# Kernel tuning notes

Measured on AMD Instinct MI355X. Metric: run time of the kernel, lower is better.

Reference implementation:

```python
import jax, jax.numpy as jnp
import numpy as np

N_NODES = 100000
N_EDGES = 3200000
IN_DIM, HID_DIM, N_CLASS = 64, 32, 20


def setup_inputs() -> dict:
    key = jax.random.key(0)
    k1, k2, k3, k4, k5, k6 = jax.random.split(key, 6)
    x = jax.random.normal(k1, (N_NODES, IN_DIM), dtype=jnp.float32)
    edge_index = jax.random.randint(k2, (2, N_EDGES), 0, N_NODES, dtype=jnp.int64)
    W1 = jax.random.normal(k3, (IN_DIM, HID_DIM), dtype=jnp.float32) / np.sqrt(IN_DIM)
    b1 = jnp.zeros((HID_DIM,), dtype=jnp.float32)
    Wout = jax.random.normal(k4, (HID_DIM, N_CLASS), dtype=jnp.float32) / np.sqrt(HID_DIM)
    bout = jnp.zeros((N_CLASS,), dtype=jnp.float32)
    return {"x": x, "edge_index": edge_index, "W1": W1, "b1": b1, "Wout": Wout, "bout": bout}


def gcn_conv(x, edge_index, W, b):
    # PyG GCNConv defaults: add self-loops, symmetric deg^{-1/2} normalization.
    n = x.shape[0]
    loop = jnp.arange(n, dtype=edge_index.dtype)
    row = jnp.concatenate([edge_index[0], loop])  # source
    col = jnp.concatenate([edge_index[1], loop])  # target
    deg = jax.ops.segment_sum(jnp.ones_like(col, dtype=x.dtype), col, num_segments=n)
    dis = jnp.where(deg > 0, deg ** -0.5, 0.0)
    norm = dis[row] * dis[col]  # [E+N]
    xw = x @ W  # [N, HID]
    msg = norm[:, None] * xw[row]  # [E+N, HID]
    agg = jax.ops.segment_sum(msg, col, num_segments=n)
    return agg + b


def reference(x, edge_index, W1, b1, Wout, bout):
    h = gcn_conv(x, edge_index, W1, b1)
    emb = jax.nn.relu(h)
    return emb @ Wout + bout
```

## Files before the change

kernel.cpp:

```cpp
#include <hip/hip_runtime.h>
#include <hip/hip_fp16.h>
#include <math.h>

#define N_NODES 100000
#define N_EDGES 3200000
#define IN_DIM 64
#define HID_DIM 32
#define N_CLASS 20

#define BKT_BITS 6
#define BKT_W    64
#define NBKT     1563
#define CAP_BKT  2560
#define HALF_W   32
#define CAP_D    1536
#define CHUNK    4096
#define EPT      16
#define NBLK_E   ((N_EDGES + CHUNK - 1) / CHUNK)
#define ENT_R    (CAP_BKT / 256)

__global__ void k_detect(const int* __restrict__ ei32, int* __restrict__ flag,
                         int* __restrict__ gcursor) {
    __shared__ int any;
    if (threadIdx.x == 0) any = 0;
    __syncthreads();
    int nz = 0;
    for (int k = threadIdx.x; k < 4096; k += blockDim.x)
        if (ei32[2 * k + 1] != 0) nz = 1;
    if (nz) atomicOr(&any, 1);
    for (int i = threadIdx.x; i < NBKT; i += blockDim.x) gcursor[i] = i * CAP_BKT;
    __syncthreads();
    if (threadIdx.x == 0) *flag = any ? 0 : 1;
}

__device__ __forceinline__ int get_idx(const int* __restrict__ ei32, int wide, int pos) {
    return wide ? ei32[2 * (long long)pos] : ei32[pos];
}

__global__ void __launch_bounds__(256, 8)
kC_scatter(const int* __restrict__ ei32, const int* __restrict__ flag,
           int* __restrict__ gcursor, unsigned int* __restrict__ pk) {
    __shared__ int lh[NBKT];
    __shared__ int lgb[NBKT];
    __shared__ int lrt[NBKT];
    int wide = *flag;
    for (int i = threadIdx.x; i < NBKT; i += blockDim.x) { lh[i] = 0; lrt[i] = 0; }
    __syncthreads();
    int base = blockIdx.x * CHUNK;
    int src[EPT], dst[EPT];
#pragma unroll
    for (int k = 0; k < EPT; ++k) {
        int e = base + k * 256 + threadIdx.x;
        if (e < N_EDGES) {
            src[k] = get_idx(ei32, wide, e);
            dst[k] = get_idx(ei32, wide, N_EDGES + e);
            atomicAdd(&lh[dst[k] >> BKT_BITS], 1);
        } else dst[k] = -1;
    }
    __syncthreads();
    for (int b = threadIdx.x; b < NBKT; b += blockDim.x)
        if (lh[b]) lgb[b] = atomicAdd(&gcursor[b], lh[b]);
    __syncthreads();
#pragma unroll
    for (int k = 0; k < EPT; ++k) {
        if (dst[k] >= 0) {
            int b = dst[k] >> BKT_BITS;
            int r = atomicAdd(&lrt[b], 1);
            int pos = lgb[b] + r;
            if (pos < (b + 1) * CAP_BKT)
                pk[pos] = ((unsigned)src[k] << BKT_BITS) | (unsigned)(dst[k] & (BKT_W - 1));
        }
    }
}

__global__ void kC1_deg(const unsigned int* __restrict__ pk, const int* __restrict__ gcursor,
                        float* __restrict__ dis) {
    __shared__ int lcnt[BKT_W];
    int b = blockIdx.x;
    int gb = b * CAP_BKT;
    int bsz = min(gcursor[b] - gb, CAP_BKT);
    if (threadIdx.x < BKT_W) lcnt[threadIdx.x] = 0;
    __syncthreads();
    for (int i = threadIdx.x; i < bsz; i += blockDim.x)
        atomicAdd(&lcnt[pk[gb + i] & (BKT_W - 1)], 1);
    __syncthreads();
    int node = b * BKT_W + threadIdx.x;
    if (threadIdx.x < BKT_W && node < N_NODES)
        dis[node] = rsqrtf((float)(lcnt[threadIdx.x] + 1));
}

__global__ void k_xw(const float* __restrict__ x, const float* __restrict__ W1,
                     const float* __restrict__ dis, __half* __restrict__ xw16) {
    __shared__ float sW[IN_DIM * HID_DIM];
    for (int i = threadIdx.x; i < IN_DIM * HID_DIM; i += blockDim.x) sW[i] = W1[i];
    __syncthreads();
    int tid = blockIdx.x * blockDim.x + threadIdx.x;
    int node = tid >> 3;
    int q = tid & 7;
    if (node >= N_NODES) return;
    const float4* xr = reinterpret_cast<const float4*>(x + (size_t)node * IN_DIM);
    float4 a = make_float4(0.f, 0.f, 0.f, 0.f);
#pragma unroll
    for (int k4 = 0; k4 < IN_DIM / 4; ++k4) {
        float4 xv = xr[k4];
        const float4 w0 = *reinterpret_cast<const float4*>(&sW[(k4 * 4 + 0) * HID_DIM + q * 4]);
        const float4 w1 = *reinterpret_cast<const float4*>(&sW[(k4 * 4 + 1) * HID_DIM + q * 4]);
        const float4 w2 = *reinterpret_cast<const float4*>(&sW[(k4 * 4 + 2) * HID_DIM + q * 4]);
        const float4 w3 = *reinterpret_cast<const float4*>(&sW[(k4 * 4 + 3) * HID_DIM + q * 4]);
        a.x += xv.x * w0.x + xv.y * w1.x + xv.z * w2.x + xv.w * w3.x;
        a.y += xv.x * w0.y + xv.y * w1.y + xv.z * w2.y + xv.w * w3.y;
        a.z += xv.x * w0.z + xv.y * w1.z + xv.z * w2.z + xv.w * w3.z;
        a.w += xv.x * w0.w + xv.y * w1.w + xv.z * w2.w + xv.w * w3.w;
    }
    float d = dis[node];
    union { __half2 h2[2]; uint2 u; } cvt;
    cvt.h2[0] = __floats2half2_rn(a.x * d, a.y * d);
    cvt.h2[1] = __floats2half2_rn(a.z * d, a.w * d);
    *reinterpret_cast<uint2*>(xw16 + (size_t)node * HID_DIM + q * 4) = cvt.u;
}

__device__ __forceinline__ void acc_row(float4& acc, uint2 u) {
    union U { unsigned u; __half2 hh; };
    U a0; a0.u = u.x; U a1; a1.u = u.y;
    float2 f0 = __half22float2(a0.hh);
    float2 f1 = __half22float2(a1.hh);
    acc.x += f0.x; acc.y += f0.y; acc.z += f1.x; acc.w += f1.y;
}

__global__ void __launch_bounds__(256, 8)
kD_gather(const unsigned int* __restrict__ pk, const int* __restrict__ gcursor,
          const float* __restrict__ dis, const __half* __restrict__ xw16,
          const float* __restrict__ b1, const float* __restrict__ Wout,
          const float* __restrict__ bout, float* __restrict__ out) {
    __shared__ int   ssrc[CAP_D];
    __shared__ int   lcnt[HALF_W], lstart[HALF_W], lrt[HALF_W];
    __shared__ int   stot;
    __shared__ float sW[HID_DIM * N_CLASS];
    __shared__ float sb1[HID_DIM];
    __shared__ float sbo[N_CLASS];
    for (int i = threadIdx.x; i < HID_DIM * N_CLASS; i += blockDim.x) sW[i] = Wout[i];
    if (threadIdx.x < HID_DIM) sb1[threadIdx.x] = b1[threadIdx.x];
    if (threadIdx.x < N_CLASS) sbo[threadIdx.x] = bout[threadIdx.x];
    if (threadIdx.x < HALF_W) { lcnt[threadIdx.x] = 0; lrt[threadIdx.x] = 0; }
    int B = blockIdx.x;
    int b = B >> 1, h = B & 1;
    int gb = b * CAP_BKT;
    int bsz = min(gcursor[b] - gb, CAP_BKT);
    __syncthreads();

    unsigned ents[ENT_R];
#pragma unroll
    for (int i = 0; i < ENT_R; ++i) {
        int idx = i * 256 + (int)threadIdx.x;
        ents[i] = (idx < bsz) ? pk[gb + idx] : 0xFFFFFFFFu;
    }
#pragma unroll
    for (int i = 0; i < ENT_R; ++i) {
        if (ents[i] != 0xFFFFFFFFu) {
            int ld = (int)(ents[i] & (BKT_W - 1));
            if ((ld >> 5) == h) atomicAdd(&lcnt[ld & (HALF_W - 1)], 1);
        }
    }
    __syncthreads();
    if (threadIdx.x < HALF_W) {
        int v = lcnt[threadIdx.x];
        int s = v;
#pragma unroll
        for (int d = 1; d < HALF_W; d <<= 1) {
            int t = __shfl_up(s, d, HALF_W);
            if ((int)(threadIdx.x & (HALF_W - 1)) >= d) s += t;
        }
        lstart[threadIdx.x] = s - v;
        if (threadIdx.x == HALF_W - 1) stot = s;
    }
    __syncthreads();
    bool fits = (stot <= CAP_D);
    if (fits) {
#pragma unroll
        for (int i = 0; i < ENT_R; ++i) {
            if (ents[i] != 0xFFFFFFFFu) {
                int ld = (int)(ents[i] & (BKT_W - 1));
                if ((ld >> 5) == h) {
                    int r = atomicAdd(&lrt[ld & (HALF_W - 1)], 1);
                    ssrc[lstart[ld & (HALF_W - 1)] + r] = (int)(ents[i] >> BKT_BITS);
                }
            }
        }
    }
    __syncthreads();

    int grp = threadIdx.x >> 3, part = threadIdx.x & 7;
    int ln = grp;
    int node = b * BKT_W + h * HALF_W + ln;
    if (node >= N_NODES) return;

    float4 acc = make_float4(0.f, 0.f, 0.f, 0.f);
    acc_row(acc, *reinterpret_cast<const uint2*>(xw16 + (size_t)node * HID_DIM + part * 4));
    float dc = dis[node];

    if (fits) {
        int s0 = lstart[ln], cnt = lcnt[ln];
        int e = s0, end = s0 + cnt;
        while (e + 8 <= end) {
            int srcs[8];
#pragma unroll
            for (int j = 0; j < 8; ++j) srcs[j] = ssrc[e + j];
            uint2 us[8];
#pragma unroll
            for (int j = 0; j < 8; ++j)
                us[j] = *reinterpret_cast<const uint2*>(xw16 + (size_t)srcs[j] * HID_DIM + part * 4);
#pragma unroll
            for (int j = 0; j < 8; ++j) acc_row(acc, us[j]);
            e += 8;
        }
        for (; e < end; ++e) {
            int src = ssrc[e];
            acc_row(acc, *reinterpret_cast<const uint2*>(xw16 + (size_t)src * HID_DIM + part * 4));
        }
    } else {
        int want = h * HALF_W + ln;
        for (int i = 0; i < bsz; ++i) {
            unsigned v = pk[gb + i];
            if ((int)(v & (BKT_W - 1)) == want)
                acc_row(acc, *reinterpret_cast<const uint2*>(xw16 + (size_t)(v >> BKT_BITS) * HID_DIM + part * 4));
        }
    }
    float e0 = fmaxf(dc * acc.x + sb1[part * 4 + 0], 0.f);
    float e1 = fmaxf(dc * acc.y + sb1[part * 4 + 1], 0.f);
    float e2 = fmaxf(dc * acc.z + sb1[part * 4 + 2], 0.f);
    float e3 = fmaxf(dc * acc.w + sb1[part * 4 + 3], 0.f);
    float o[N_CLASS];
#pragma unroll
    for (int cl = 0; cl < N_CLASS; ++cl) {
        o[cl] = e0 * sW[(part * 4 + 0) * N_CLASS + cl]
              + e1 * sW[(part * 4 + 1) * N_CLASS + cl]
              + e2 * sW[(part * 4 + 2) * N_CLASS + cl]
              + e3 * sW[(part * 4 + 3) * N_CLASS + cl];
    }
#pragma unroll
    for (int m = 1; m < 8; m <<= 1) {
#pragma unroll
        for (int cl = 0; cl < N_CLASS; ++cl) o[cl] += __shfl_xor(o[cl], m, 64);
    }
    if (part < 5) {
        float4 w = make_float4(o[part * 4 + 0] + sbo[part * 4 + 0],
                               o[part * 4 + 1] + sbo[part * 4 + 1],
                               o[part * 4 + 2] + sbo[part * 4 + 2],
                               o[part * 4 + 3] + sbo[part * 4 + 3]);
        *reinterpret_cast<float4*>(out + (size_t)node * N_CLASS + part * 4) = w;
    }
}

extern "C" void kernel_launch(void* const* d_in, const int* in_sizes, int n_in,
                              void* d_out, int out_size, void* d_ws, size_t ws_size,
                              hipStream_t stream) {
    const float* x    = (const float*)d_in[0];
    const int*   ei32 = (const int*)d_in[1];
    const float* W1   = (const float*)d_in[2];
    const float* b1   = (const float*)d_in[3];
    const float* Wout = (const float*)d_in[4];
    const float* bout = (const float*)d_in[5];
    float* out = (float*)d_out;

    __half*       xw16    = (__half*)d_ws;
    unsigned int* pk      = (unsigned int*)((char*)d_ws + (size_t)N_NODES * HID_DIM * 2);
    int*          gcursor = (int*)(pk + (size_t)NBKT * CAP_BKT);
    float*        dis     = (float*)(gcursor + NBKT);
    int*          flag    = (int*)(dis + N_NODES);

    k_detect<<<1, 256, 0, stream>>>(ei32, flag, gcursor);
    kC_scatter<<<NBLK_E, 256, 0, stream>>>(ei32, flag, gcursor, pk);
    kC1_deg<<<NBKT, 256, 0, stream>>>(pk, gcursor, dis);
    k_xw<<<(N_NODES * 8 + 255) / 256, 256, 0, stream>>>(x, W1, dis, xw16);
    kD_gather<<<2 * NBKT, 256, 0, stream>>>(pk, gcursor, dis, xw16, b1, Wout, bout, out);
}
```

Before: 137.5 us.

## Split edge bucketing into two-pass radix scatter via coarse super-buckets

```diff
diff --git a/kernel.cpp b/kernel.cpp
--- a/kernel.cpp
+++ b/kernel.cpp
@@ -14,13 +14,18 @@
 #define CAP_BKT  2560
 #define HALF_W   32
 #define CAP_D    1536
-#define CHUNK    4096
-#define EPT      16
-#define NBLK_E   ((N_EDGES + CHUNK - 1) / CHUNK)
 #define ENT_R    (CAP_BKT / 256)
 
+#define SUP_SHIFT 12
+#define NS       25
+#define CAP_S    132000
+#define CH1      2048
+#define NBLK1    ((N_EDGES + CH1 - 1) / CH1)
+#define CH2      4096
+#define BPS      ((CAP_S + CH2 - 1) / CH2)
+
 __global__ void k_detect(const int* __restrict__ ei32, int* __restrict__ flag,
-                         int* __restrict__ gcursor) {
+                         int* __restrict__ scursor, int* __restrict__ gcursor) {
     __shared__ int any;
     if (threadIdx.x == 0) any = 0;
     __syncthreads();
@@ -29,6 +34,7 @@
         if (ei32[2 * k + 1] != 0) nz = 1;
     if (nz) atomicOr(&any, 1);
     for (int i = threadIdx.x; i < NBKT; i += blockDim.x) gcursor[i] = i * CAP_BKT;
+    if (threadIdx.x < NS) scursor[threadIdx.x] = threadIdx.x * CAP_S;
     __syncthreads();
     if (threadIdx.x == 0) *flag = any ? 0 : 1;
 }
@@ -37,38 +43,78 @@
     return wide ? ei32[2 * (long long)pos] : ei32[pos];
 }
 
-__global__ void __launch_bounds__(256, 8)
-kC_scatter(const int* __restrict__ ei32, const int* __restrict__ flag,
-           int* __restrict__ gcursor, unsigned int* __restrict__ pk) {
-    __shared__ int lh[NBKT];
-    __shared__ int lgb[NBKT];
-    __shared__ int lrt[NBKT];
+__global__ void __launch_bounds__(512, 4)
+kS1(const int* __restrict__ ei32, const int* __restrict__ flag,
+    int* __restrict__ scursor, unsigned int* __restrict__ sp) {
+    __shared__ int lh[NS], lgb[NS], lrt[NS];
     int wide = *flag;
-    for (int i = threadIdx.x; i < NBKT; i += blockDim.x) { lh[i] = 0; lrt[i] = 0; }
-    __syncthreads();
-    int base = blockIdx.x * CHUNK;
-    int src[EPT], dst[EPT];
-#pragma unroll
-    for (int k = 0; k < EPT; ++k) {
-        int e = base + k * 256 + threadIdx.x;
+    if (threadIdx.x < NS) { lh[threadIdx.x] = 0; lrt[threadIdx.x] = 0; }
+    __syncthreads();
+    int base = blockIdx.x * CH1;
+    int src[4], dst[4];
+#pragma unroll
+    for (int k = 0; k < 4; ++k) {
+        int e = base + k * 512 + (int)threadIdx.x;
         if (e < N_EDGES) {
             src[k] = get_idx(ei32, wide, e);
             dst[k] = get_idx(ei32, wide, N_EDGES + e);
-            atomicAdd(&lh[dst[k] >> BKT_BITS], 1);
+            atomicAdd(&lh[dst[k] >> SUP_SHIFT], 1);
         } else dst[k] = -1;
     }
     __syncthreads();
-    for (int b = threadIdx.x; b < NBKT; b += blockDim.x)
-        if (lh[b]) lgb[b] = atomicAdd(&gcursor[b], lh[b]);
-    __syncthreads();
-#pragma unroll
-    for (int k = 0; k < EPT; ++k) {
+    if (threadIdx.x < NS && lh[threadIdx.x])
+        lgb[threadIdx.x] = atomicAdd(&scursor[threadIdx.x], lh[threadIdx.x]);
+    __syncthreads();
+#pragma unroll
+    for (int k = 0; k < 4; ++k) {
         if (dst[k] >= 0) {
-            int b = dst[k] >> BKT_BITS;
-            int r = atomicAdd(&lrt[b], 1);
-            int pos = lgb[b] + r;
+            int s = dst[k] >> SUP_SHIFT;
+            int r = atomicAdd(&lrt[s], 1);
+            int pos = lgb[s] + r;
+            if (pos < (s + 1) * CAP_S)
+                sp[pos] = ((unsigned)src[k] << SUP_SHIFT) |
+                          (unsigned)(dst[k] & ((1 << SUP_SHIFT) - 1));
+        }
+    }
+}
+
+__global__ void __launch_bounds__(512, 4)
+kS2(const unsigned int* __restrict__ sp, const int* __restrict__ scursor,
+    int* __restrict__ gcursor, unsigned int* __restrict__ pk) {
+    __shared__ int lh[BKT_W], lgb[BKT_W], lrt[BKT_W];
+    int s = blockIdx.x / BPS;
+    int j = blockIdx.x % BPS;
+    int sbase = s * CAP_S;
+    int scount = min(scursor[s] - sbase, CAP_S);
+    int start = j * CH2;
+    if (start >= scount) return;
+    int end = min(start + CH2, scount);
+    if (threadIdx.x < BKT_W) { lh[threadIdx.x] = 0; lrt[threadIdx.x] = 0; }
+    __syncthreads();
+    unsigned ent[8]; int fb[8];
+#pragma unroll
+    for (int k = 0; k < 8; ++k) {
+        int i = start + k * 512 + (int)threadIdx.x;
+        if (i < end) {
+            ent[k] = sp[sbase + i];
+            fb[k] = (int)((ent[k] & ((1u << SUP_SHIFT) - 1)) >> BKT_BITS);
+            atomicAdd(&lh[fb[k]], 1);
+        } else fb[k] = -1;
+    }
+    __syncthreads();
+    if (threadIdx.x < BKT_W && lh[threadIdx.x]) {
+        int b = s * BKT_W + (int)threadIdx.x;
+        if (b < NBKT) lgb[threadIdx.x] = atomicAdd(&gcursor[b], lh[threadIdx.x]);
+    }
+    __syncthreads();
+#pragma unroll
+    for (int k = 0; k < 8; ++k) {
+        if (fb[k] >= 0) {
+            int b = s * BKT_W + fb[k];
+            int r = atomicAdd(&lrt[fb[k]], 1);
+            int pos = lgb[fb[k]] + r;
             if (pos < (b + 1) * CAP_BKT)
-                pk[pos] = ((unsigned)src[k] << BKT_BITS) | (unsigned)(dst[k] & (BKT_W - 1));
+                pk[pos] = ((ent[k] >> SUP_SHIFT) << BKT_BITS) | (ent[k] & (BKT_W - 1));
         }
     }
 }
@@ -262,14 +308,17 @@
     const float* bout = (const float*)d_in[5];
     float* out = (float*)d_out;
 
+    unsigned int* sp      = (unsigned int*)d_ws;
     __half*       xw16    = (__half*)d_ws;
-    unsigned int* pk      = (unsigned int*)((char*)d_ws + (size_t)N_NODES * HID_DIM * 2);
+    unsigned int* pk      = sp + (size_t)NS * CAP_S;
     int*          gcursor = (int*)(pk + (size_t)NBKT * CAP_BKT);
-    float*        dis     = (float*)(gcursor + NBKT);
+    int*          scursor = gcursor + NBKT;
+    float*        dis     = (float*)(scursor + NS);
     int*          flag    = (int*)(dis + N_NODES);
 
-    k_detect<<<1, 256, 0, stream>>>(ei32, flag, gcursor);
-    kC_scatter<<<NBLK_E, 256, 0, stream>>>(ei32, flag, gcursor, pk);
+    k_detect<<<1, 256, 0, stream>>>(ei32, flag, scursor, gcursor);
+    kS1<<<NBLK1, 512, 0, stream>>>(ei32, flag, scursor, sp);
+    kS2<<<NS * BPS, 512, 0, stream>>>(sp, scursor, gcursor, pk);
     kC1_deg<<<NBKT, 256, 0, stream>>>(pk, gcursor, dis);
     k_xw<<<(N_NODES * 8 + 255) / 256, 256, 0, stream>>>(x, W1, dis, xw16);
     kD_gather<<<2 * NBKT, 256, 0, stream>>>(pk, gcursor, dis, xw16, b1, Wout, bout, out);
```

Measured after the change: 123.8 us. 10.0% less time.
